# Performance work log

Measured on AMD Instinct MI355X. Metric: run time of the kernel, lower is better.

The kernel has to match this reference:

```python
import jax, jax.numpy as jnp
import numpy as np

B, S, H = 2, 8192, 1024
NUM_HEADS = 16
HEAD_DIM = H // NUM_HEADS
KERNEL = 7
DILATION = 1
SCALE = 1.0 / np.sqrt(HEAD_DIM)


def setup_inputs() -> dict:
    key = jax.random.key(0)
    ks = jax.random.split(key, 9)
    init = 0.02
    return {
        "hidden_states": jax.random.normal(ks[0], (B, S, H), dtype=jnp.float32),
        "w_q": jax.random.normal(ks[1], (H, H), dtype=jnp.float32) * init,
        "b_q": jnp.zeros((H,), dtype=jnp.float32),
        "w_k": jax.random.normal(ks[2], (H, H), dtype=jnp.float32) * init,
        "b_k": jnp.zeros((H,), dtype=jnp.float32),
        "w_v": jax.random.normal(ks[3], (H, H), dtype=jnp.float32) * init,
        "b_v": jnp.zeros((H,), dtype=jnp.float32),
        "w_o": jax.random.normal(ks[4], (H, H), dtype=jnp.float32) * init,
        "b_o": jnp.zeros((H,), dtype=jnp.float32),
    }


def reference(hidden_states, w_q, b_q, w_k, b_k, w_v, b_v, w_o, b_o):
    b, s, h = hidden_states.shape
    # QKV projections (weights stored [in, out])
    q = hidden_states @ w_q + b_q
    k = hidden_states @ w_k + b_k
    v = hidden_states @ w_v + b_v
    # [B, nH, S, hd]
    q = q.reshape(b, s, NUM_HEADS, HEAD_DIM).transpose(0, 2, 1, 3)
    k = k.reshape(b, s, NUM_HEADS, HEAD_DIM).transpose(0, 2, 1, 3)
    v = v.reshape(b, s, NUM_HEADS, HEAD_DIM).transpose(0, 2, 1, 3)

    # Neighborhood window indices: for query i, keys at i + (j - K//2)*dilation
    offsets = (jnp.arange(KERNEL) - KERNEL // 2) * DILATION  # [K]
    idx = jnp.arange(s)[:, None] + offsets[None, :]          # [S, K]
    valid = (idx >= 0) & (idx < s)                           # [S, K]
    idx_c = jnp.clip(idx, 0, s - 1)

    k_win = k[:, :, idx_c, :]  # [B, nH, S, K, hd]
    v_win = v[:, :, idx_c, :]  # [B, nH, S, K, hd]

    scores = jnp.einsum('bhsd,bhskd->bhsk', q, k_win) * SCALE
    scores = jnp.where(valid[None, None], scores, -jnp.inf)
    attn = jax.nn.softmax(scores, axis=-1)                   # [B, nH, S, K]
    out = jnp.einsum('bhsk,bhskd->bhsd', attn, v_win)        # [B, nH, S, hd]

    out = out.transpose(0, 2, 1, 3).reshape(b, s, h)
    return out @ w_o + b_o
```

## Files before the change

### kernel.cpp

```cpp
#include <hip/hip_runtime.h>


typedef __bf16 bf16x8 __attribute__((ext_vector_type(8)));
typedef float f32x4 __attribute__((ext_vector_type(4)));
typedef int int4v __attribute__((ext_vector_type(4)));
typedef __attribute__((address_space(1))) void as1_void;
typedef __attribute__((address_space(3))) void as3_void;

__device__ __forceinline__ float bf2f(unsigned short u) {
    union { unsigned int u; float f; } c;
    c.u = ((unsigned int)u) << 16;
    return c.f;
}
__device__ __forceinline__ unsigned short f2bf(float f) {
    union { float f; unsigned int u; } c;
    c.f = f;
    unsigned int u = c.u;
    u += 0x7fffu + ((u >> 16) & 1u);
    return (unsigned short)(u >> 16);
}

__global__ __launch_bounds__(256) void prep(
    const float* __restrict__ X, const float* __restrict__ w0,
    const float* __restrict__ w1, const float* __restrict__ w2,
    const float* __restrict__ w3, const float* __restrict__ bq,
    const float* __restrict__ bk, const float* __restrict__ bv,
    unsigned short* __restrict__ Xb, unsigned short* __restrict__ t0,
    unsigned short* __restrict__ t3, float* __restrict__ biasQ) {
    __shared__ unsigned short tile[32][33];
    const int bid = blockIdx.x;
    if (bid < 16384) {
        int i = bid * 256 + threadIdx.x;
        float4 v = ((const float4*)X)[i];
        ushort4 o;
        o.x = f2bf(v.x); o.y = f2bf(v.y); o.z = f2bf(v.z); o.w = f2bf(v.w);
        ((ushort4*)Xb)[i] = o;
    } else if (bid < 20480) {
        const int t = bid - 16384;
        const int z = t >> 10;
        const int rem = t & 1023;
        const float* W = (z == 0) ? w0 : (z == 1) ? w1 : (z == 2) ? w2 : w3;
        unsigned short* Wt = (z == 3) ? t3 : t0 + (size_t)z * 1048576;
        const int c0 = (rem & 31) * 32;
        const int r0 = (rem >> 5) * 32;
        const int tx = threadIdx.x & 31;
        const int ty = threadIdx.x >> 5;
#pragma unroll
        for (int i = 0; i < 32; i += 8)
            tile[ty + i][tx] = f2bf(W[(size_t)(r0 + ty + i) * 1024 + c0 + tx]);
        __syncthreads();
#pragma unroll
        for (int i = 0; i < 32; i += 8)
            Wt[(size_t)(c0 + ty + i) * 1024 + r0 + tx] = tile[tx][ty + i];
    } else {
        int i = (bid - 20480) * 256 + threadIdx.x;
        if (i < 3072)
            biasQ[i] = (i < 1024) ? bq[i] : ((i < 2048) ? bk[i - 1024] : bv[i - 2048]);
    }
}

__global__ __launch_bounds__(512, 2) void gemm_qkv8(
    const unsigned short* __restrict__ A, const unsigned short* __restrict__ Bt,
    const float* __restrict__ bias, unsigned short* __restrict__ Cb,
    unsigned short* __restrict__ Vt) {
    constexpr int K = 1024;
    constexpr int NT = 16;
    __shared__ unsigned short smem[65536];
    const int tid  = threadIdx.x;
    const int lane = tid & 63;
    const int wave = tid >> 6;
    const int quad = lane >> 4;
    const int mr   = lane & 15;

    const int id  = blockIdx.x;
    const int swz = (id & 7) * 96 + (id >> 3);
    const int bm  = (swz / 12) * 256;
    const int bn  = (swz % 12) * 256;
    const int wm  = (wave >> 2) * 128;
    const int wn  = (wave & 3) * 64;

    const int r0 = tid >> 3;
    const int g8 = ((lane & 7) ^ ((lane >> 3) & 7)) * 8;
    const unsigned short* srcA = A  + (size_t)(bm + r0) * K + g8;
    const unsigned short* srcB = Bt + (size_t)(bn + r0) * K + g8;

    auto stage = [&](const unsigned short* gb, int ldsByte, int kt) {
#pragma unroll
        for (int l = 0; l < 2; ++l)
            __builtin_amdgcn_global_load_lds(
                (const as1_void*)(gb + (size_t)l * 65536 + kt),
                (as3_void*)((char*)smem + ldsByte + l * 8192 + tid * 16),
                16, 0, 0);
    };

    stage(srcA,          0,     0);
    stage(srcA + 131072, 16384, 0);
    stage(srcB,          32768, 0);
    stage(srcB + 131072, 49152, 0);
    stage(srcB,          65536 + 32768, 64);
    stage(srcB + 131072, 65536 + 49152, 64);
    asm volatile("s_waitcnt vmcnt(4)" ::: "memory");
    asm volatile("s_barrier" ::: "memory");

    const int aRow = (wm + mr) * 64;
    const int bRow = 16384 + (wn + mr) * 64;
    const int c8_0 = ((0 * 4 + quad) ^ (mr & 7)) * 8;
    const int c8_1 = ((1 * 4 + quad) ^ (mr & 7)) * 8;

    f32x4 acc[8][4] = {};

    for (int t = 0; t < NT; ++t) {
        const int bufS  = (t & 1) << 15;
        const int nbufB = ((t + 1) & 1) << 16;
        const int cbufB = (t & 1) << 16;
        const int ktA = (t + 1 < NT ? t + 1 : NT - 1) * 64;
        const int ktB = (t + 2 < NT ? t + 2 : NT - 1) * 64;

        bf16x8 afL[4][2], bA[2][2], bB[2][2];
#pragma unroll
        for (int i = 0; i < 4; ++i) {
            afL[i][0] = *(const bf16x8*)(smem + bufS + aRow + i * 1024 + c8_0);
            afL[i][1] = *(const bf16x8*)(smem + bufS + aRow + i * 1024 + c8_1);
        }
#pragma unroll
        for (int j = 0; j < 2; ++j) {
            bA[j][0] = *(const bf16x8*)(smem + bufS + bRow + j * 1024 + c8_0);
            bA[j][1] = *(const bf16x8*)(smem + bufS + bRow + j * 1024 + c8_1);
        }
#pragma unroll
        for (int j = 0; j < 2; ++j) {
            bB[j][0] = *(const bf16x8*)(smem + bufS + bRow + (j + 2) * 1024 + c8_0);
            bB[j][1] = *(const bf16x8*)(smem + bufS + bRow + (j + 2) * 1024 + c8_1);
        }
        stage(srcA, nbufB, ktA);
        __builtin_amdgcn_s_setprio(1);
#pragma unroll
        for (int i = 0; i < 4; ++i)
#pragma unroll
            for (int j = 0; j < 2; ++j) {
                acc[i][j] = __builtin_amdgcn_mfma_f32_16x16x32_bf16(afL[i][0], bA[j][0], acc[i][j], 0, 0, 0);
                acc[i][j] = __builtin_amdgcn_mfma_f32_16x16x32_bf16(afL[i][1], bA[j][1], acc[i][j], 0, 0, 0);
            }
        __builtin_amdgcn_s_setprio(0);
        asm volatile("s_barrier" ::: "memory");

        stage(srcA + 131072, nbufB + 16384, ktA);
        __builtin_amdgcn_s_setprio(1);
#pragma unroll
        for (int i = 0; i < 4; ++i)
#pragma unroll
            for (int j = 0; j < 2; ++j) {
                acc[i][j + 2] = __builtin_amdgcn_mfma_f32_16x16x32_bf16(afL[i][0], bB[j][0], acc[i][j + 2], 0, 0, 0);
                acc[i][j + 2] = __builtin_amdgcn_mfma_f32_16x16x32_bf16(afL[i][1], bB[j][1], acc[i][j + 2], 0, 0, 0);
            }
        __builtin_amdgcn_s_setprio(0);
        asm volatile("s_barrier" ::: "memory");

        bf16x8 afH[4][2];
#pragma unroll
        for (int i = 0; i < 4; ++i) {
            afH[i][0] = *(const bf16x8*)(smem + bufS + aRow + (i + 4) * 1024 + c8_0);
            afH[i][1] = *(const bf16x8*)(smem + bufS + aRow + (i + 4) * 1024 + c8_1);
        }
        stage(srcB, cbufB + 32768, ktB);
        __builtin_amdgcn_s_setprio(1);
#pragma unroll
        for (int i = 0; i < 4; ++i)
#pragma unroll
            for (int j = 0; j < 2; ++j) {
                acc[i + 4][j + 2] = __builtin_amdgcn_mfma_f32_16x16x32_bf16(afH[i][0], bB[j][0], acc[i + 4][j + 2], 0, 0, 0);
                acc[i + 4][j + 2] = __builtin_amdgcn_mfma_f32_16x16x32_bf16(afH[i][1], bB[j][1], acc[i + 4][j + 2], 0, 0, 0);
            }
        __builtin_amdgcn_s_setprio(0);
        asm volatile("s_barrier" ::: "memory");

        stage(srcB + 131072, cbufB + 49152, ktB);
        __builtin_amdgcn_s_setprio(1);
#pragma unroll
        for (int i = 0; i < 4; ++i)
#pragma unroll
            for (int j = 0; j < 2; ++j) {
                acc[i + 4][j] = __builtin_amdgcn_mfma_f32_16x16x32_bf16(afH[i][0], bA[j][0], acc[i + 4][j], 0, 0, 0);
                acc[i + 4][j] = __builtin_amdgcn_mfma_f32_16x16x32_bf16(afH[i][1], bA[j][1], acc[i + 4][j], 0, 0, 0);
            }
        __builtin_amdgcn_s_setprio(0);
        asm volatile("s_waitcnt vmcnt(4)" ::: "memory");
        asm volatile("s_barrier" ::: "memory");
    }

    asm volatile("s_waitcnt vmcnt(0) lgkmcnt(0)" ::: "memory");
    asm volatile("s_barrier" ::: "memory");

    unsigned short* ep = smem + wave * 8192;
    if (bn < 2048) {
#pragma unroll
        for (int h = 0; h < 2; ++h) {
#pragma unroll
            for (int j = 0; j < 4; ++j) {
                const float bvv = bias[bn + wn + j * 16 + mr];
#pragma unroll
                for (int i = 0; i < 4; ++i)
#pragma unroll
                    for (int r = 0; r < 4; ++r)
                        ep[(i * 16 + quad * 4 + r) * 68 + j * 16 + mr] =
                            f2bf(acc[h * 4 + i][j][r] + bvv);
            }
#pragma unroll
            for (int p = 0; p < 8; ++p) {
                const int row = p * 8 + (lane >> 3);
                const int gr = lane & 7;
                int4v v = *(const int4v*)(ep + row * 68 + gr * 8);
                *(int4v*)(Cb + (size_t)(bm + wm + h * 64 + row) * 2048 + bn + wn + gr * 8) = v;
            }
        }
    } else {
        const int bb = (bm + wm) >> 13;
        const int sb = (bm + wm) & 8191;
        const size_t vrow0 = (size_t)bb * 8388608 + (size_t)(bn - 2048 + wn) * 8192 + sb;
#pragma unroll
        for (int h = 0; h < 2; ++h) {
#pragma unroll
            for (int j = 0; j < 4; ++j) {
                const float bvv = bias[bn + wn + j * 16 + mr];
#pragma unroll
                for (int i = 0; i < 4; ++i)
#pragma unroll
                    for (int r = 0; r < 4; ++r)
                        ep[(j * 16 + mr) * 68 + i * 16 + quad * 4 + r] =
                            f2bf(acc[h * 4 + i][j][r] + bvv);
            }
#pragma unroll
            for (int p = 0; p < 8; ++p) {
                const int d = p * 8 + (lane >> 3);
                const int gr = lane & 7;
                int4v v = *(const int4v*)(ep + d * 68 + gr * 8);
                *(int4v*)(Vt + vrow0 + (size_t)d * 8192 + h * 64 + gr * 8) = v;
            }
        }
    }
}

template <int MODE, int MT>
__device__ __forceinline__ void gemm_body(
    const unsigned short* __restrict__ A, const unsigned short* __restrict__ Bt,
    const float* __restrict__ bias, float* __restrict__ Cf,
    unsigned short* __restrict__ Cb, unsigned short* __restrict__ Vt,
    int N, int K) {
    __shared__ unsigned short smem[MT * 2048 + 8192];
    const int tid = threadIdx.x;
    const int lane = tid & 63;
    const int wave = tid >> 6;
    const int bm = blockIdx.y * (MT * 32);
    const int bn = blockIdx.x * 128;
    const int wm = (wave >> 1) * (MT * 16);
    const int wn = (wave & 1) * 64;
    const int quad = lane >> 4;
    const int mr = lane & 15;

    const unsigned short* gA[MT];
    const unsigned short* gB[4];
    char* lA[MT];
    char* lB[4];
#pragma unroll
    for (int k = 0; k < MT; ++k) {
        const int q = (k * 4 + wave) * 64 + lane;
        const int row = q >> 3;
        const int c8 = (q & 7) ^ (row & 7);
        gA[k] = A + (size_t)(bm + row) * K + c8 * 8;
        lA[k] = (char*)smem + (size_t)(k * 4 + wave) * 1024;
    }
#pragma unroll
    for (int k = 0; k < 4; ++k) {
        const int q = (k * 4 + wave) * 64 + lane;
        const int row = q >> 3;
        const int c8 = (q & 7) ^ (row & 7);
        gB[k] = Bt + (size_t)(bn + row) * K + c8 * 8;
        lB[k] = (char*)smem + (size_t)MT * 4096 + (size_t)(k * 4 + wave) * 1024;
    }

    f32x4 acc[MT][4] = {};

    for (int kt = 0; kt < K; kt += 64) {
#pragma unroll
        for (int k = 0; k < MT; ++k) {
            __builtin_amdgcn_global_load_lds((as1_void*)gA[k], (as3_void*)lA[k], 16, 0, 0);
            gA[k] += 64;
        }
#pragma unroll
        for (int k = 0; k < 4; ++k) {
            __builtin_amdgcn_global_load_lds((as1_void*)gB[k], (as3_void*)lB[k], 16, 0, 0);
            gB[k] += 64;
        }
        __syncthreads();

#pragma unroll
        for (int kk = 0; kk < 2; ++kk) {
            const int c8 = (kk * 4 + quad) ^ (mr & 7);
            bf16x8 af[MT], bfr[4];
#pragma unroll
            for (int i = 0; i < MT; ++i)
                af[i] = *(const bf16x8*)(smem + (wm + i * 16 + mr) * 64 + c8 * 8);
#pragma unroll
            for (int j = 0; j < 4; ++j)
                bfr[j] = *(const bf16x8*)(smem + MT * 2048 + (wn + j * 16 + mr) * 64 + c8 * 8);
#pragma unroll
            for (int i = 0; i < MT; ++i)
#pragma unroll
                for (int j = 0; j < 4; ++j)
                    acc[i][j] = __builtin_amdgcn_mfma_f32_16x16x32_bf16(
                        af[i], bfr[j], acc[i][j], 0, 0, 0);
        }
        __syncthreads();
    }

    if (MODE == 0) {
        float* epf = (float*)smem + wave * 1280;
#pragma unroll
        for (int j = 0; j < 4; ++j) {
            const int gcol0 = bn + wn + j * 16;
            const float bv = bias[gcol0 + mr];
#pragma unroll
            for (int h2 = 0; h2 < MT / 4; ++h2) {
#pragma unroll
                for (int i2 = 0; i2 < 4; ++i2)
#pragma unroll
                    for (int r = 0; r < 4; ++r)
                        epf[(i2 * 16 + quad * 4 + r) * 20 + mr] = acc[h2 * 4 + i2][j][r] + bv;
#pragma unroll
                for (int p = 0; p < 4; ++p) {
                    const int dr = p * 16 + (lane >> 2);
                    const int ch = lane & 3;
                    f32x4 v = *(const f32x4*)(epf + dr * 20 + ch * 4);
                    *(f32x4*)(Cf + (size_t)(bm + wm + h2 * 64 + dr) * N + gcol0 + ch * 4) = v;
                }
            }
        }
    }
}

__global__ __launch_bounds__(256, 4) void gemm_out(
    const unsigned short* __restrict__ A, const unsigned short* __restrict__ Bt,
    const float* __restrict__ bias, float* __restrict__ Cf, int N, int K) {
    gemm_body<0, 4>(A, Bt, bias, Cf, nullptr, nullptr, N, K);
}

__global__ __launch_bounds__(256) void attn_mfma(
    const unsigned short* __restrict__ QK, const unsigned short* __restrict__ Vt,
    unsigned short* __restrict__ out) {
    __shared__ unsigned short sP[4][64 * 104];
    const int tid = threadIdx.x;
    const int lane = tid & 63;
    const int wave = tid >> 6;
    const int quad = lane >> 4;
    const int cc = lane & 15;
    const int w = blockIdx.x * 4 + wave;
    const int b = w >> 11;
    const int h = (w >> 7) & 15;
    const int st = w & 127;
    const int s0 = st << 6;
    const int win0 = s0 - 8;
    const size_t tokBase = (size_t)b * 8192;
    unsigned short* P = sP[wave];

    {
        int4v z = {0, 0, 0, 0};
#pragma unroll
        for (int i = 0; i < 13; ++i)
            *(int4v*)(P + i * 512 + lane * 8) = z;
    }

    f32x4 accS[4][5] = {};
#pragma unroll
    for (int kc = 0; kc < 2; ++kc) {
        bf16x8 qf[4], kf[5];
#pragma unroll
        for (int mt = 0; mt < 4; ++mt)
            qf[mt] = *(const bf16x8*)(QK + (tokBase + s0 + mt * 16 + cc) * 2048
                                      + h * 64 + kc * 32 + quad * 8);
#pragma unroll
        for (int nt = 0; nt < 5; ++nt) {
            int row = win0 + nt * 16 + cc;
            row = row < 0 ? 0 : (row > 8191 ? 8191 : row);
            kf[nt] = *(const bf16x8*)(QK + (tokBase + row) * 2048
                                      + 1024 + h * 64 + kc * 32 + quad * 8);
        }
#pragma unroll
        for (int mt = 0; mt < 4; ++mt)
#pragma unroll
            for (int nt = 0; nt < 5; ++nt)
                accS[mt][nt] = __builtin_amdgcn_mfma_f32_16x16x32_bf16(
                    qf[mt], kf[nt], accS[mt][nt], 0, 0, 0);
    }

    const float NEG = -__builtin_inff();
#pragma unroll
    for (int mt = 0; mt < 4; ++mt) {
#pragma unroll
        for (int r = 0; r < 4; ++r) {
            const int mrow = mt * 16 + quad * 4 + r;
            float v[5];
#pragma unroll
            for (int nt = 0; nt < 5; ++nt) {
                const int k = nt * 16 + cc;
                const int rel = k - mrow;
                const int sidx = win0 + k;
                const bool ok = (rel >= 5) & (rel <= 11) & (sidx >= 0) & (sidx < 8192);
                v[nt] = ok ? accS[mt][nt][r] * 0.125f : NEG;
            }
            float mx = v[0];
#pragma unroll
            for (int nt = 1; nt < 5; ++nt) mx = fmaxf(mx, v[nt]);
#pragma unroll
            for (int off = 8; off >= 1; off >>= 1) mx = fmaxf(mx, __shfl_xor(mx, off));
            float p[5], sum = 0.f;
#pragma unroll
            for (int nt = 0; nt < 5; ++nt) {
                p[nt] = __builtin_amdgcn_exp2f((v[nt] - mx) * 1.44269504f);
                sum += p[nt];
            }
#pragma unroll
            for (int off = 8; off >= 1; off >>= 1) sum += __shfl_xor(sum, off);
            const float inv = __builtin_amdgcn_rcpf(sum);
#pragma unroll
            for (int nt = 0; nt < 5; ++nt)
                P[mrow * 104 + nt * 16 + cc] = f2bf(p[nt] * inv);
        }
    }

    f32x4 accO[4][4] = {};
#pragma unroll
    for (int kc = 0; kc < 3; ++kc) {
        bf16x8 pf[4], vf[4];
#pragma unroll
        for (int mt = 0; mt < 4; ++mt)
            pf[mt] = *(const bf16x8*)(P + (mt * 16 + cc) * 104 + kc * 32 + quad * 8);
        {
            int pos = win0 + kc * 32 + quad * 8;
            pos = pos < 0 ? 0 : (pos > 8184 ? 8184 : pos);
#pragma unroll
            for (int nt = 0; nt < 4; ++nt)
                vf[nt] = *(const bf16x8*)(Vt + ((size_t)(b * 16 + h) * 64 + nt * 16 + cc) * 8192 + pos);
        }
#pragma unroll
        for (int mt = 0; mt < 4; ++mt)
#pragma unroll
            for (int nt = 0; nt < 4; ++nt)
                accO[mt][nt] = __builtin_amdgcn_mfma_f32_16x16x32_bf16(
                    pf[mt], vf[nt], accO[mt][nt], 0, 0, 0);
    }

#pragma unroll
    for (int mt = 0; mt < 4; ++mt)
#pragma unroll
        for (int nt = 0; nt < 4; ++nt)
#pragma unroll
            for (int r = 0; r < 4; ++r)
                P[(mt * 16 + quad * 4 + r) * 72 + nt * 16 + cc] = f2bf(accO[mt][nt][r]);

#pragma unroll
    for (int pass = 0; pass < 8; ++pass) {
        const int row = pass * 8 + (lane >> 3);
        const int ch = lane & 7;
        int4v vv = *(const int4v*)(P + row * 72 + ch * 8);
        *(int4v*)(out + (tokBase + s0 + row) * 1024 + h * 64 + ch * 8) = vv;
    }
}

extern "C" void kernel_launch(void* const* d_in, const int* in_sizes, int n_in,
                              void* d_out, int out_size, void* d_ws, size_t ws_size,
                              hipStream_t stream) {
    (void)in_sizes; (void)n_in; (void)out_size; (void)ws_size;
    const float* X  = (const float*)d_in[0];
    const float* wq = (const float*)d_in[1];
    const float* bq = (const float*)d_in[2];
    const float* wk = (const float*)d_in[3];
    const float* bk = (const float*)d_in[4];
    const float* wv = (const float*)d_in[5];
    const float* bv = (const float*)d_in[6];
    const float* wo = (const float*)d_in[7];
    const float* bo = (const float*)d_in[8];
    float* out = (float*)d_out;

    char* ws = (char*)d_ws;
    unsigned short* Xb    = (unsigned short*)(ws);
    unsigned short* WtQKV = (unsigned short*)(ws + 33554432);
    unsigned short* WtO   = (unsigned short*)(ws + 39845888);
    unsigned short* QK    = (unsigned short*)(ws + 41943040);
    unsigned short* Vt    = (unsigned short*)(ws + 109051904);
    unsigned short* AttnO = (unsigned short*)(ws + 142606336);
    float*          biasQ = (float*)(ws + 176160768);

    prep<<<20492, 256, 0, stream>>>(X, wq, wk, wv, wo, bq, bk, bv,
                                    Xb, WtQKV, WtO, biasQ);

    gemm_qkv8<<<768, 512, 0, stream>>>(Xb, WtQKV, biasQ, QK, Vt);

    attn_mfma<<<1024, 256, 0, stream>>>(QK, Vt, AttnO);

    gemm_out<<<dim3(8, 128), 256, 0, stream>>>(AttnO, WtO, bo, out, 1024, 1024);
}
```

Before: 313.9 us.

## Replace MFMA attention with per-thread VALU attention over unified QKV layout

The QKV GEMM now writes Q, K and V into one token-major [tokens, 3072] bf16 buffer, dropping the transposed V epilogue. The MFMA-based attention, which computed a padded 64x80 score tile per wave and wasted most of the work on masked entries, is replaced by a scalar VALU kernel where each thread handles one (token, head) pair and computes exactly 7 dot products and a weighted V sum. The aim is to cut the wasted windowed work and simplify memory access. The cost is heavy per-thread register use (64-float q and output arrays) and redundant K/V loads across neighbouring tokens, which rely on the cache.

```diff
diff --git a/kernel.cpp b/kernel.cpp
--- a/kernel.cpp
+++ b/kernel.cpp
@@ -4,6 +4,7 @@
 typedef __bf16 bf16x8 __attribute__((ext_vector_type(8)));
 typedef float f32x4 __attribute__((ext_vector_type(4)));
 typedef int int4v __attribute__((ext_vector_type(4)));
+typedef unsigned short u16x8 __attribute__((ext_vector_type(8)));
 typedef __attribute__((address_space(1))) void as1_void;
 typedef __attribute__((address_space(3))) void as3_void;
 
@@ -61,8 +62,7 @@
 
 __global__ __launch_bounds__(512, 2) void gemm_qkv8(
     const unsigned short* __restrict__ A, const unsigned short* __restrict__ Bt,
-    const float* __restrict__ bias, unsigned short* __restrict__ Cb,
-    unsigned short* __restrict__ Vt) {
+    const float* __restrict__ bias, unsigned short* __restrict__ Cb) {
     constexpr int K = 1024;
     constexpr int NT = 16;
     __shared__ unsigned short smem[65536];
@@ -192,51 +192,95 @@
     asm volatile("s_barrier" ::: "memory");
 
     unsigned short* ep = smem + wave * 8192;
-    if (bn < 2048) {
-#pragma unroll
-        for (int h = 0; h < 2; ++h) {
-#pragma unroll
-            for (int j = 0; j < 4; ++j) {
-                const float bvv = bias[bn + wn + j * 16 + mr];
-#pragma unroll
-                for (int i = 0; i < 4; ++i)
-#pragma unroll
-                    for (int r = 0; r < 4; ++r)
-                        ep[(i * 16 + quad * 4 + r) * 68 + j * 16 + mr] =
-                            f2bf(acc[h * 4 + i][j][r] + bvv);
-            }
-#pragma unroll
-            for (int p = 0; p < 8; ++p) {
-                const int row = p * 8 + (lane >> 3);
-                const int gr = lane & 7;
-                int4v v = *(const int4v*)(ep + row * 68 + gr * 8);
-                *(int4v*)(Cb + (size_t)(bm + wm + h * 64 + row) * 2048 + bn + wn + gr * 8) = v;
-            }
-        }
-    } else {
-        const int bb = (bm + wm) >> 13;
-        const int sb = (bm + wm) & 8191;
-        const size_t vrow0 = (size_t)bb * 8388608 + (size_t)(bn - 2048 + wn) * 8192 + sb;
-#pragma unroll
-        for (int h = 0; h < 2; ++h) {
-#pragma unroll
-            for (int j = 0; j < 4; ++j) {
-                const float bvv = bias[bn + wn + j * 16 + mr];
-#pragma unroll
-                for (int i = 0; i < 4; ++i)
-#pragma unroll
-                    for (int r = 0; r < 4; ++r)
-                        ep[(j * 16 + mr) * 68 + i * 16 + quad * 4 + r] =
-                            f2bf(acc[h * 4 + i][j][r] + bvv);
-            }
-#pragma unroll
-            for (int p = 0; p < 8; ++p) {
-                const int d = p * 8 + (lane >> 3);
-                const int gr = lane & 7;
-                int4v v = *(const int4v*)(ep + d * 68 + gr * 8);
-                *(int4v*)(Vt + vrow0 + (size_t)d * 8192 + h * 64 + gr * 8) = v;
-            }
-        }
+#pragma unroll
+    for (int h = 0; h < 2; ++h) {
+#pragma unroll
+        for (int j = 0; j < 4; ++j) {
+            const float bvv = bias[bn + wn + j * 16 + mr];
+#pragma unroll
+            for (int i = 0; i < 4; ++i)
+#pragma unroll
+                for (int r = 0; r < 4; ++r)
+                    ep[(i * 16 + quad * 4 + r) * 68 + j * 16 + mr] =
+                        f2bf(acc[h * 4 + i][j][r] + bvv);
+        }
+#pragma unroll
+        for (int p = 0; p < 8; ++p) {
+            const int row = p * 8 + (lane >> 3);
+            const int gr = lane & 7;
+            int4v v = *(const int4v*)(ep + row * 68 + gr * 8);
+            *(int4v*)(Cb + (size_t)(bm + wm + h * 64 + row) * 3072 + bn + wn + gr * 8) = v;
+        }
+    }
+}
+
+__global__ __launch_bounds__(256) void attn_valu(
+    const unsigned short* __restrict__ QKV, unsigned short* __restrict__ out) {
+    const int tid = threadIdx.x;
+    const int h   = tid & 15;
+    const int tl  = tid >> 4;
+    const int tok = blockIdx.x * 16 + tl;
+    const int s   = tok & 8191;
+    const size_t base = (size_t)tok * 3072 + h * 64;
+
+    float qf[64];
+#pragma unroll
+    for (int i = 0; i < 8; ++i) {
+        u16x8 qv = *(const u16x8*)(QKV + base + i * 8);
+#pragma unroll
+        for (int e = 0; e < 8; ++e) qf[i * 8 + e] = bf2f(qv[e]);
+    }
+
+    float sc[7];
+#pragma unroll
+    for (int j = 0; j < 7; ++j) {
+        const int ks = s + j - 3;
+        const bool ok = (ks >= 0) & (ks < 8192);
+        const int kc = ks < 0 ? 0 : (ks > 8191 ? 8191 : ks);
+        const size_t kb = base + (size_t)(kc - s) * 3072 + 1024;
+        float acc = 0.f;
+#pragma unroll
+        for (int i = 0; i < 8; ++i) {
+            u16x8 kv = *(const u16x8*)(QKV + kb + i * 8);
+#pragma unroll
+            for (int e = 0; e < 8; ++e) acc += qf[i * 8 + e] * bf2f(kv[e]);
+        }
+        sc[j] = ok ? acc * 0.125f : -__builtin_inff();
+    }
+
+    float mx = sc[0];
+#pragma unroll
+    for (int j = 1; j < 7; ++j) mx = fmaxf(mx, sc[j]);
+    float p[7], sum = 0.f;
+#pragma unroll
+    for (int j = 0; j < 7; ++j) {
+        p[j] = __builtin_amdgcn_exp2f((sc[j] - mx) * 1.44269504f);
+        sum += p[j];
+    }
+    const float inv = __builtin_amdgcn_rcpf(sum);
+
+    float o[64] = {};
+#pragma unroll
+    for (int j = 0; j < 7; ++j) {
+        const int ks = s + j - 3;
+        const int kc = ks < 0 ? 0 : (ks > 8191 ? 8191 : ks);
+        const size_t vb = base + (size_t)(kc - s) * 3072 + 2048;
+        const float pj = p[j] * inv;
+#pragma unroll
+        for (int i = 0; i < 8; ++i) {
+            u16x8 vv = *(const u16x8*)(QKV + vb + i * 8);
+#pragma unroll
+            for (int e = 0; e < 8; ++e) o[i * 8 + e] += pj * bf2f(vv[e]);
+        }
+    }
+
+    const size_t dst = (size_t)tok * 1024 + h * 64;
+#pragma unroll
+    for (int i = 0; i < 8; ++i) {
+        u16x8 ov;
+#pragma unroll
+        for (int e = 0; e < 8; ++e) ov[e] = f2bf(o[i * 8 + e]);
+        *(u16x8*)(out + dst + i * 8) = ov;
     }
 }
 
@@ -244,7 +288,6 @@
 __device__ __forceinline__ void gemm_body(
     const unsigned short* __restrict__ A, const unsigned short* __restrict__ Bt,
     const float* __restrict__ bias, float* __restrict__ Cf,
-    unsigned short* __restrict__ Cb, unsigned short* __restrict__ Vt,
     int N, int K) {
     __shared__ unsigned short smem[MT * 2048 + 8192];
     const int tid = threadIdx.x;
@@ -341,129 +384,7 @@
 __global__ __launch_bounds__(256, 4) void gemm_out(
     const unsigned short* __restrict__ A, const unsigned short* __restrict__ Bt,
     const float* __restrict__ bias, float* __restrict__ Cf, int N, int K) {
-    gemm_body<0, 4>(A, Bt, bias, Cf, nullptr, nullptr, N, K);
-}
-
-__global__ __launch_bounds__(256) void attn_mfma(
-    const unsigned short* __restrict__ QK, const unsigned short* __restrict__ Vt,
-    unsigned short* __restrict__ out) {
-    __shared__ unsigned short sP[4][64 * 104];
-    const int tid = threadIdx.x;
-    const int lane = tid & 63;
-    const int wave = tid >> 6;
-    const int quad = lane >> 4;
-    const int cc = lane & 15;
-    const int w = blockIdx.x * 4 + wave;
-    const int b = w >> 11;
-    const int h = (w >> 7) & 15;
-    const int st = w & 127;
-    const int s0 = st << 6;
-    const int win0 = s0 - 8;
-    const size_t tokBase = (size_t)b * 8192;
-    unsigned short* P = sP[wave];
-
-    {
-        int4v z = {0, 0, 0, 0};
-#pragma unroll
-        for (int i = 0; i < 13; ++i)
-            *(int4v*)(P + i * 512 + lane * 8) = z;
-    }
-
-    f32x4 accS[4][5] = {};
-#pragma unroll
-    for (int kc = 0; kc < 2; ++kc) {
-        bf16x8 qf[4], kf[5];
-#pragma unroll
-        for (int mt = 0; mt < 4; ++mt)
-            qf[mt] = *(const bf16x8*)(QK + (tokBase + s0 + mt * 16 + cc) * 2048
-                                      + h * 64 + kc * 32 + quad * 8);
-#pragma unroll
-        for (int nt = 0; nt < 5; ++nt) {
-            int row = win0 + nt * 16 + cc;
-            row = row < 0 ? 0 : (row > 8191 ? 8191 : row);
-            kf[nt] = *(const bf16x8*)(QK + (tokBase + row) * 2048
-                                      + 1024 + h * 64 + kc * 32 + quad * 8);
-        }
-#pragma unroll
-        for (int mt = 0; mt < 4; ++mt)
-#pragma unroll
-            for (int nt = 0; nt < 5; ++nt)
-                accS[mt][nt] = __builtin_amdgcn_mfma_f32_16x16x32_bf16(
-                    qf[mt], kf[nt], accS[mt][nt], 0, 0, 0);
-    }
-
-    const float NEG = -__builtin_inff();
-#pragma unroll
-    for (int mt = 0; mt < 4; ++mt) {
-#pragma unroll
-        for (int r = 0; r < 4; ++r) {
-            const int mrow = mt * 16 + quad * 4 + r;
-            float v[5];
-#pragma unroll
-            for (int nt = 0; nt < 5; ++nt) {
-                const int k = nt * 16 + cc;
-                const int rel = k - mrow;
-                const int sidx = win0 + k;
-                const bool ok = (rel >= 5) & (rel <= 11) & (sidx >= 0) & (sidx < 8192);
-                v[nt] = ok ? accS[mt][nt][r] * 0.125f : NEG;
-            }
-            float mx = v[0];
-#pragma unroll
-            for (int nt = 1; nt < 5; ++nt) mx = fmaxf(mx, v[nt]);
-#pragma unroll
-            for (int off = 8; off >= 1; off >>= 1) mx = fmaxf(mx, __shfl_xor(mx, off));
-            float p[5], sum = 0.f;
-#pragma unroll
-            for (int nt = 0; nt < 5; ++nt) {
-                p[nt] = __builtin_amdgcn_exp2f((v[nt] - mx) * 1.44269504f);
-                sum += p[nt];
-            }
-#pragma unroll
-            for (int off = 8; off >= 1; off >>= 1) sum += __shfl_xor(sum, off);
-            const float inv = __builtin_amdgcn_rcpf(sum);
-#pragma unroll
-            for (int nt = 0; nt < 5; ++nt)
-                P[mrow * 104 + nt * 16 + cc] = f2bf(p[nt] * inv);
-        }
-    }
-
-    f32x4 accO[4][4] = {};
-#pragma unroll
-    for (int kc = 0; kc < 3; ++kc) {
-        bf16x8 pf[4], vf[4];
-#pragma unroll
-        for (int mt = 0; mt < 4; ++mt)
-            pf[mt] = *(const bf16x8*)(P + (mt * 16 + cc) * 104 + kc * 32 + quad * 8);
-        {
-            int pos = win0 + kc * 32 + quad * 8;
-            pos = pos < 0 ? 0 : (pos > 8184 ? 8184 : pos);
-#pragma unroll
-            for (int nt = 0; nt < 4; ++nt)
-                vf[nt] = *(const bf16x8*)(Vt + ((size_t)(b * 16 + h) * 64 + nt * 16 + cc) * 8192 + pos);
-        }
-#pragma unroll
-        for (int mt = 0; mt < 4; ++mt)
-#pragma unroll
-            for (int nt = 0; nt < 4; ++nt)
-                accO[mt][nt] = __builtin_amdgcn_mfma_f32_16x16x32_bf16(
-                    pf[mt], vf[nt], accO[mt][nt], 0, 0, 0);
-    }
-
-#pragma unroll
-    for (int mt = 0; mt < 4; ++mt)
-#pragma unroll
-        for (int nt = 0; nt < 4; ++nt)
-#pragma unroll
-            for (int r = 0; r < 4; ++r)
-                P[(mt * 16 + quad * 4 + r) * 72 + nt * 16 + cc] = f2bf(accO[mt][nt][r]);
-
-#pragma unroll
-    for (int pass = 0; pass < 8; ++pass) {
-        const int row = pass * 8 + (lane >> 3);
-        const int ch = lane & 7;
-        int4v vv = *(const int4v*)(P + row * 72 + ch * 8);
-        *(int4v*)(out + (tokBase + s0 + row) * 1024 + h * 64 + ch * 8) = vv;
-    }
+    gemm_body<0, 4>(A, Bt, bias, Cf, N, K);
 }
 
 extern "C" void kernel_launch(void* const* d_in, const int* in_sizes, int n_in,
@@ -485,17 +406,16 @@
     unsigned short* Xb    = (unsigned short*)(ws);
     unsigned short* WtQKV = (unsigned short*)(ws + 33554432);
     unsigned short* WtO   = (unsigned short*)(ws + 39845888);
-    unsigned short* QK    = (unsigned short*)(ws + 41943040);
-    unsigned short* Vt    = (unsigned short*)(ws + 109051904);
+    unsigned short* QKV   = (unsigned short*)(ws + 41943040);
     unsigned short* AttnO = (unsigned short*)(ws + 142606336);
     float*          biasQ = (float*)(ws + 176160768);
 
     prep<<<20492, 256, 0, stream>>>(X, wq, wk, wv, wo, bq, bk, bv,
                                     Xb, WtQKV, WtO, biasQ);
 
-    gemm_qkv8<<<768, 512, 0, stream>>>(Xb, WtQKV, biasQ, QK, Vt);
-
-    attn_mfma<<<1024, 256, 0, stream>>>(QK, Vt, AttnO);
+    gemm_qkv8<<<768, 512, 0, stream>>>(Xb, WtQKV, biasQ, QKV);
+
+    attn_valu<<<1024, 256, 0, stream>>>(QKV, AttnO);
 
     gemm_out<<<dim3(8, 128), 256, 0, stream>>>(AttnO, WtO, bo, out, 1024, 1024);
 }
```

Result: slower. 354.9 us (+13.1%).
